# Kernel tuning notes

Measured on AMD Instinct MI355X. Metric: run time of the kernel, lower is better.

The kernel has to match this reference:

```python
import jax, jax.numpy as jnp
import numpy as np

HEADS = 12
DIM = 768
DH = DIM // HEADS


def setup_inputs() -> dict:
    key = jax.random.key(0)
    k1, k2 = jax.random.split(key)
    z = jax.random.normal(k1, (4, 2048, DIM), dtype=jnp.float32)
    # nn.Linear(dim, 3*dim, bias=False): weight shape [3*dim, dim], y = z @ W.T
    W_qkv = jax.random.normal(k2, (3 * DIM, DIM), dtype=jnp.float32) * (1.0 / np.sqrt(DIM))
    return {"z": z, "W_qkv": W_qkv}


def reference(z, W_qkv):
    b, n, d = z.shape
    qkv = jnp.einsum('bnd,ed->bne', z, W_qkv)  # [b, n, 3*dim]
    # last dim layout is (headNum, m, Dh) per the einops pattern '(headNum m Dh)'
    qkv = qkv.reshape(b, n, HEADS, 3, DH)
    q = jnp.transpose(qkv[:, :, :, 0, :], (0, 2, 1, 3))  # [b, h, n, Dh]
    k = jnp.transpose(qkv[:, :, :, 1, :], (0, 2, 1, 3))
    v = jnp.transpose(qkv[:, :, :, 2, :], (0, 2, 1, 3))
    scores = jnp.einsum('bhqd,bhkd->bhqk', q, k) / np.sqrt(DH).astype(np.float32)
    A = jax.nn.softmax(scores, axis=-1)  # full [b, h, n, n] matrix, as in source
    out = jnp.einsum('bhqk,bhkd->bhqd', A, v)  # [b, h, n, Dh]
    return jnp.transpose(out, (0, 2, 1, 3)).reshape(b, n, d)
```

## Files before the change

### kernel.cpp

```cpp
#include <hip/hip_runtime.h>
#include <hip/hip_bf16.h>
#include <stdint.h>


typedef __attribute__((ext_vector_type(8))) short bf8_t;
typedef __attribute__((ext_vector_type(4))) float f4_t;

__device__ __forceinline__ unsigned short f2bf(float f) {
  union { float f; unsigned u; } x; x.f = f;
  return (unsigned short)((x.u + 0x7fffu + ((x.u >> 16) & 1u)) >> 16);
}
__device__ __forceinline__ unsigned cvt_pk_bf16(float lo, float hi) {
  unsigned r;
  asm("v_cvt_pk_bf16_f32 %0, %1, %2" : "=v"(r) : "v"(lo), "v"(hi));
  return r;
}
__device__ __forceinline__ void gload_lds16(const void* g, void* l) {
  __builtin_amdgcn_global_load_lds(
      (const __attribute__((address_space(1))) void*)g,
      (__attribute__((address_space(3))) void*)l, 16, 0, 0);
}

__global__ __launch_bounds__(256) void cvt_kernel(
    const float* __restrict__ Z, const float* __restrict__ W,
    unsigned short* __restrict__ Zb)
{
  const int idx = blockIdx.x * 256 + threadIdx.x;
  const float* src;
  unsigned short* dst;
  int c;
  if (idx < 786432) { src = Z; dst = Zb; c = idx; }
  else              { src = W; dst = Zb + 6291456; c = idx - 786432; }
  const float4 a0 = *(const float4*)(src + (size_t)c * 8);
  const float4 a1 = *(const float4*)(src + (size_t)c * 8 + 4);
  uint4 pk = { cvt_pk_bf16(a0.x, a0.y), cvt_pk_bf16(a0.z, a0.w),
               cvt_pk_bf16(a1.x, a1.y), cvt_pk_bf16(a1.z, a1.w) };
  *(uint4*)(dst + (size_t)c * 8) = pk;
}

__global__ __launch_bounds__(256, 3) void qkv_gemm_kernel(
    const unsigned short* __restrict__ Zb, const unsigned short* __restrict__ Wb,
    unsigned short* __restrict__ qb, unsigned short* __restrict__ kb,
    unsigned short* __restrict__ vt)
{
  __shared__ __align__(16) unsigned short As[128 * 64];
  __shared__ __align__(16) unsigned short Bs[128 * 64];

  const int tid = threadIdx.x;
  const int w    = tid >> 6;
  const int lane = tid & 63;
  const int g    = lane >> 4;
  const int l15  = lane & 15;
  const int bid0 = blockIdx.y * 18 + blockIdx.x;
  const int bid  = (bid0 & 7) * 144 + (bid0 >> 3);
  const int m0 = (bid / 18) * 128;
  const int n0 = (bid % 18) * 128;
  const int wr = w >> 1, wc = w & 1;

  const int arow = w * 32 + (lane >> 3);
  const int achk = ((lane & 7) ^ (lane >> 3)) * 8;
  const unsigned short* za = Zb + (size_t)(m0 + arow) * 768 + achk;
  const unsigned short* wa = Wb + (size_t)(n0 + arow) * 768 + achk;
  unsigned short* const lza = As + w * 32 * 64;
  unsigned short* const lwa = Bs + w * 32 * 64;

  const f4_t zf = {0.f, 0.f, 0.f, 0.f};
  f4_t acc[4][4];
#pragma unroll
  for (int m = 0; m < 4; ++m)
#pragma unroll
    for (int n = 0; n < 4; ++n) acc[m][n] = zf;

  for (int ks = 0; ks < 12; ++ks) {
    __syncthreads();
#pragma unroll
    for (int r = 0; r < 4; ++r) {
      gload_lds16(za + r * 8 * 768, lza + r * 512);
      gload_lds16(wa + r * 8 * 768, lwa + r * 512);
    }
    za += 64; wa += 64;
    __syncthreads();

#pragma unroll
    for (int s = 0; s < 2; ++s) {
      bf8_t af[4], bfr[4];
#pragma unroll
      for (int m = 0; m < 4; ++m) {
        const int row = wr * 64 + m * 16 + l15;
        af[m] = *(const bf8_t*)(As + row * 64 + (((s * 4 + g) ^ (row & 7)) * 8));
      }
#pragma unroll
      for (int n = 0; n < 4; ++n) {
        const int row = wc * 64 + n * 16 + l15;
        bfr[n] = *(const bf8_t*)(Bs + row * 64 + (((s * 4 + g) ^ (row & 7)) * 8));
      }
      __builtin_amdgcn_s_setprio(1);
#pragma unroll
      for (int m = 0; m < 4; ++m)
#pragma unroll
        for (int n = 0; n < 4; ++n)
          acc[m][n] = __builtin_amdgcn_mfma_f32_16x16x32_bf16(af[m], bfr[n], acc[m][n], 0, 0, 0);
      __builtin_amdgcn_s_setprio(0);
    }
  }

  const float QSCALE = 0.18033688011112042f;
#pragma unroll
  for (int m = 0; m < 4; ++m) {
    const int gi  = m0 + wr * 64 + m * 16 + g * 4;
    const int b   = gi >> 11;
    const int tok = gi & 2047;
#pragma unroll
    for (int n = 0; n < 4; ++n) {
      const int e0  = n0 + wc * 64 + n * 16;
      const int h   = e0 / 192;
      const int rem = e0 - h * 192;
      const int mm  = rem >> 6;
      const int dh  = (rem & 63) + l15;
      if (mm == 2) {
        uint2 pk = { cvt_pk_bf16(acc[m][n][0], acc[m][n][1]),
                     cvt_pk_bf16(acc[m][n][2], acc[m][n][3]) };
        const int pos = ((tok >> 5) & 1) * 32 + ((tok >> 2) & 3) * 8
                      + ((tok >> 4) & 1) * 4;
        const size_t vaddr = ((size_t)(b * 12 + h) * 32 + (tok >> 6)) * 4096
                           + dh * 64 + pos;
        *(uint2*)(vt + vaddr) = pk;
      } else {
        unsigned short* buf = mm ? kb : qb;
        const float sc = mm ? 1.0f : QSCALE;
        const size_t base = ((size_t)((b * 12 + h) * 2048 + tok)) * 64 + dh;
#pragma unroll
        for (int j = 0; j < 4; ++j)
          buf[base + (size_t)j * 64] = f2bf(acc[m][n][j] * sc);
      }
    }
  }
}

template <int SPLIT>
__global__ __launch_bounds__(256, 3) void attn_body(
    const unsigned short* __restrict__ qb, const unsigned short* __restrict__ kb,
    const unsigned short* __restrict__ vt, float* __restrict__ out0,
    float* __restrict__ out1, float* __restrict__ lsb)
{
  __shared__ __align__(16) unsigned short Ks[2][64 * 64];
  __shared__ __align__(16) unsigned short Vs[2][64 * 64];

  const int NT = SPLIT ? 16 : 32;
  const int bid = blockIdx.x;
  int bh, qt, half;
  if (SPLIT) {
    const int nb = (bid & 7) * 192 + (bid >> 3);
    qt = nb & 15;
    half = (nb >> 4) & 1;
    bh = nb >> 5;
  } else {
    const int nb = (bid & 7) * 96 + (bid >> 3);
    qt = nb & 15;
    half = 0;
    bh = nb >> 4;
  }
  const int tid = threadIdx.x;
  const int w    = tid >> 6;
  const int lane = tid & 63;
  const int g    = lane >> 4;
  const int l15  = lane & 15;

  const unsigned short* Qh  = qb + (size_t)bh * 2048 * 64;
  const unsigned short* Kh  = kb + (size_t)bh * 2048 * 64 + (size_t)half * 16 * 4096;
  const unsigned short* VTh = vt + (size_t)bh * 32 * 4096 + (size_t)half * 16 * 4096;

  const int qbase = qt * 128 + w * 32;

  bf8_t qfr[2][2];
#pragma unroll
  for (int qq = 0; qq < 2; ++qq)
#pragma unroll
    for (int s = 0; s < 2; ++s)
      qfr[qq][s] = *(const bf8_t*)(Qh + (size_t)(qbase + qq * 16 + l15) * 64 + s * 32 + g * 8);

  const int xk   = l15 & 7;
  const int offA = l15 * 64 + ((g) ^ xk) * 8;
  const int offB = l15 * 64 + ((4 + g) ^ xk) * 8;

  const size_t dmaoff = (size_t)(w * 16 + (lane >> 3)) * 64
                      + ((lane & 7) ^ (lane >> 3)) * 8;
  const unsigned short* ksrc = Kh + dmaoff;
  const unsigned short* vsrc = VTh + dmaoff;
  const int ldsoff = w * 16 * 64;

  gload_lds16(ksrc,                 &Ks[0][ldsoff]);
  gload_lds16(ksrc + 8 * 64,        &Ks[0][ldsoff + 8 * 64]);
  gload_lds16(vsrc,                 &Vs[0][ldsoff]);
  gload_lds16(vsrc + 8 * 64,        &Vs[0][ldsoff + 8 * 64]);
  gload_lds16(ksrc + 4096,          &Ks[1][ldsoff]);
  gload_lds16(ksrc + 4096 + 8 * 64, &Ks[1][ldsoff + 8 * 64]);
  gload_lds16(vsrc + 4096,          &Vs[1][ldsoff]);
  gload_lds16(vsrc + 4096 + 8 * 64, &Vs[1][ldsoff + 8 * 64]);
  __syncthreads();

  const unsigned short* kdma = ksrc + 2 * 4096;
  const unsigned short* vdma = vsrc + 2 * 4096;

  const f4_t m16 = {-16.f, -16.f, -16.f, -16.f};
  const f4_t zf  = {0.f, 0.f, 0.f, 0.f};
  f4_t accO[2][4];
  float lsumP[2] = {0.f, 0.f};
#pragma unroll
  for (int qq = 0; qq < 2; ++qq)
#pragma unroll
    for (int nf = 0; nf < 4; ++nf) accO[qq][nf] = zf;

  for (int t = 0; t < NT; ++t) {
    const int cur = t & 1;
    const unsigned short* pK = &Ks[cur][0];
    const unsigned short* pV = &Vs[cur][0];

    bf8_t ka[4][2];
#pragma unroll
    for (int kf = 0; kf < 4; ++kf) {
      ka[kf][0] = *(const bf8_t*)(pK + offA + kf * 1024);
      ka[kf][1] = *(const bf8_t*)(pK + offB + kf * 1024);
    }
    bf8_t vfr[2][4];
#pragma unroll
    for (int nf = 0; nf < 4; ++nf) {
      vfr[0][nf] = *(const bf8_t*)(pV + offA + nf * 1024);
      vfr[1][nf] = *(const bf8_t*)(pV + offB + nf * 1024);
    }

    __syncthreads();

    if (t < NT - 2) {
      gload_lds16(kdma,          &Ks[cur][ldsoff]);
      gload_lds16(kdma + 8 * 64, &Ks[cur][ldsoff + 8 * 64]);
      gload_lds16(vdma,          &Vs[cur][ldsoff]);
      gload_lds16(vdma + 8 * 64, &Vs[cur][ldsoff + 8 * 64]);
      kdma += 4096; vdma += 4096;
    }

    f4_t accS0[4], accS1[4];
    __builtin_amdgcn_s_setprio(1);
#pragma unroll
    for (int kf = 0; kf < 4; ++kf) {
      f4_t a = __builtin_amdgcn_mfma_f32_16x16x32_bf16(ka[kf][0], qfr[0][0], m16, 0, 0, 0);
      accS0[kf] = __builtin_amdgcn_mfma_f32_16x16x32_bf16(ka[kf][1], qfr[0][1], a, 0, 0, 0);
    }
#pragma unroll
    for (int kf = 0; kf < 4; ++kf) {
      f4_t a = __builtin_amdgcn_mfma_f32_16x16x32_bf16(ka[kf][0], qfr[1][0], m16, 0, 0, 0);
      accS1[kf] = __builtin_amdgcn_mfma_f32_16x16x32_bf16(ka[kf][1], qfr[1][1], a, 0, 0, 0);
    }
    __builtin_amdgcn_s_setprio(0);

#pragma unroll
    for (int qq = 0; qq < 2; ++qq) {
      const f4_t* accS = qq ? accS1 : accS0;
      union { bf8_t v[2]; unsigned uw[8]; } P8;
      float ps = 0.f;
#pragma unroll
      for (int kf = 0; kf < 4; ++kf) {
        const float p0 = __builtin_amdgcn_exp2f(accS[kf][0]);
        const float p1 = __builtin_amdgcn_exp2f(accS[kf][1]);
        const float p2 = __builtin_amdgcn_exp2f(accS[kf][2]);
        const float p3 = __builtin_amdgcn_exp2f(accS[kf][3]);
        ps += (p0 + p1) + (p2 + p3);
        P8.uw[kf * 2]     = cvt_pk_bf16(p0, p1);
        P8.uw[kf * 2 + 1] = cvt_pk_bf16(p2, p3);
      }
      lsumP[qq] += ps;

      __builtin_amdgcn_s_setprio(1);
#pragma unroll
      for (int kk = 0; kk < 2; ++kk)
#pragma unroll
        for (int nf = 0; nf < 4; ++nf)
          accO[qq][nf] = __builtin_amdgcn_mfma_f32_16x16x32_bf16(P8.v[kk], vfr[kk][nf], accO[qq][nf], 0, 0, 0);
      __builtin_amdgcn_s_setprio(0);
    }
  }

  const int b = bh / 12, h = bh - (bh / 12) * 12;
  float* const outP = (SPLIT && half) ? out1 : out0;
#pragma unroll
  for (int qq = 0; qq < 2; ++qq) {
    float ls = lsumP[qq];
    ls += __shfl_xor(ls, 16);
    ls += __shfl_xor(ls, 32);
    if (SPLIT) {
      if (g == 0)
        lsb[((size_t)half * 48 + bh) * 2048 + qbase + qq * 16 + l15] = ls;
#pragma unroll
      for (int nf = 0; nf < 4; ++nf)
#pragma unroll
        for (int j = 0; j < 4; ++j) {
          const int qrow = qbase + qq * 16 + g * 4 + j;
          outP[((size_t)(b * 2048 + qrow)) * 768 + h * 64 + nf * 16 + l15] = accO[qq][nf][j];
        }
    } else {
      const float rl = 1.0f / ls;
      f4_t lv;
#pragma unroll
      for (int j = 0; j < 4; ++j) lv[j] = __shfl(rl, g * 4 + j);
#pragma unroll
      for (int nf = 0; nf < 4; ++nf)
#pragma unroll
        for (int j = 0; j < 4; ++j) {
          const int qrow = qbase + qq * 16 + g * 4 + j;
          outP[((size_t)(b * 2048 + qrow)) * 768 + h * 64 + nf * 16 + l15] = accO[qq][nf][j] * lv[j];
        }
    }
  }
}

__global__ __launch_bounds__(256) void combine_kernel(
    float* __restrict__ out, const float* __restrict__ P1,
    const float* __restrict__ lsb)
{
  const int tid = blockIdx.x * 256 + threadIdx.x;
  const int row = tid >> 3;
  const int dh0 = (tid & 7) * 8;
  const int bh  = row >> 11;
  const int tok = row & 2047;
  const int b   = bh / 12, h = bh - (bh / 12) * 12;

  const float ls = lsb[row] + lsb[(size_t)48 * 2048 + row];
  const float rl = 1.0f / ls;

  const size_t base = ((size_t)(b * 2048 + tok)) * 768 + h * 64 + dh0;
  float4 a0 = *(const float4*)(out + base);
  float4 a1 = *(const float4*)(out + base + 4);
  const float4 b0 = *(const float4*)(P1 + base);
  const float4 b1 = *(const float4*)(P1 + base + 4);
  a0.x = (a0.x + b0.x) * rl; a0.y = (a0.y + b0.y) * rl;
  a0.z = (a0.z + b0.z) * rl; a0.w = (a0.w + b0.w) * rl;
  a1.x = (a1.x + b1.x) * rl; a1.y = (a1.y + b1.y) * rl;
  a1.z = (a1.z + b1.z) * rl; a1.w = (a1.w + b1.w) * rl;
  *(float4*)(out + base)     = a0;
  *(float4*)(out + base + 4) = a1;
}

extern "C" void kernel_launch(void* const* d_in, const int* in_sizes, int n_in,
                              void* d_out, int out_size, void* d_ws, size_t ws_size,
                              hipStream_t stream) {
  (void)in_sizes; (void)n_in; (void)out_size;
  const float* Z = (const float*)d_in[0];
  const float* W = (const float*)d_in[1];
  float* out = (float*)d_out;

  unsigned short* qb = (unsigned short*)d_ws;
  unsigned short* kb = qb + (size_t)48 * 2048 * 64;
  unsigned short* vt = kb + (size_t)48 * 2048 * 64;

  float* P1  = (float*)(vt + (size_t)48 * 32 * 4096);
  float* lsb = P1 + (size_t)48 * 2048 * 64;
  const size_t WS_NEEDED = ((size_t)48 * 2048 * 64 * 2) * 3
                         + (size_t)48 * 2048 * 64 * 4
                         + (size_t)2 * 48 * 2048 * 4;

  unsigned short* Zb = (unsigned short*)d_out;
  unsigned short* Wb = Zb + (size_t)8192 * 768;

  cvt_kernel<<<dim3(3936), 256, 0, stream>>>(Z, W, Zb);
  qkv_gemm_kernel<<<dim3(18, 64), 256, 0, stream>>>(Zb, Wb, qb, kb, vt);

  if (ws_size >= WS_NEEDED) {
    attn_body<1><<<dim3(1536), 256, 0, stream>>>(qb, kb, vt, out, P1, lsb);
    combine_kernel<<<dim3(3072), 256, 0, stream>>>(out, P1, lsb);
  } else {
    attn_body<0><<<dim3(768), 256, 0, stream>>>(qb, kb, vt, out, nullptr, nullptr);
  }
}
```

Baseline: 118.4 us.

## Double per-warp query rows and restructure K/V prefetch to issue before compute

Each warp now handles 64 query rows (4 fragments) instead of 32, so each block covers 256 queries and the grid is halved. Every K/V tile loaded into LDS is therefore reused across twice as many queries. The pipeline changes from a two-tile-ahead prefetch placed after a mid-iteration barrier to a one-tile-ahead prefetch into the other buffer at the top of each iteration, with a single barrier at the end. The trade-off is higher register pressure from the larger accumulators and P buffers under launch_bounds(256,3), which may cause spills or lower occupancy, and a smaller grid of 768 blocks.

```diff
diff --git a/kernel.cpp b/kernel.cpp
--- a/kernel.cpp
+++ b/kernel.cpp
@@ -150,15 +150,11 @@
   const int bid = blockIdx.x;
   int bh, qt, half;
   if (SPLIT) {
-    const int nb = (bid & 7) * 192 + (bid >> 3);
-    qt = nb & 15;
-    half = (nb >> 4) & 1;
-    bh = nb >> 5;
+    const int nb = (bid & 7) * 96 + (bid >> 3);
+    bh = nb >> 4; qt = (nb >> 1) & 7; half = nb & 1;
   } else {
-    const int nb = (bid & 7) * 96 + (bid >> 3);
-    qt = nb & 15;
-    half = 0;
-    bh = nb >> 4;
+    const int nb = (bid & 7) * 48 + (bid >> 3);
+    bh = nb >> 3; qt = nb & 7; half = 0;
   }
   const int tid = threadIdx.x;
   const int w    = tid >> 6;
@@ -170,11 +166,11 @@
   const unsigned short* Kh  = kb + (size_t)bh * 2048 * 64 + (size_t)half * 16 * 4096;
   const unsigned short* VTh = vt + (size_t)bh * 32 * 4096 + (size_t)half * 16 * 4096;
 
-  const int qbase = qt * 128 + w * 32;
-
-  bf8_t qfr[2][2];
-#pragma unroll
-  for (int qq = 0; qq < 2; ++qq)
+  const int qbase = qt * 256 + w * 64;
+
+  bf8_t qfr[4][2];
+#pragma unroll
+  for (int qq = 0; qq < 4; ++qq)
 #pragma unroll
     for (int s = 0; s < 2; ++s)
       qfr[qq][s] = *(const bf8_t*)(Qh + (size_t)(qbase + qq * 16 + l15) * 64 + s * 32 + g * 8);
@@ -189,32 +185,36 @@
   const unsigned short* vsrc = VTh + dmaoff;
   const int ldsoff = w * 16 * 64;
 
-  gload_lds16(ksrc,                 &Ks[0][ldsoff]);
-  gload_lds16(ksrc + 8 * 64,        &Ks[0][ldsoff + 8 * 64]);
-  gload_lds16(vsrc,                 &Vs[0][ldsoff]);
-  gload_lds16(vsrc + 8 * 64,        &Vs[0][ldsoff + 8 * 64]);
-  gload_lds16(ksrc + 4096,          &Ks[1][ldsoff]);
-  gload_lds16(ksrc + 4096 + 8 * 64, &Ks[1][ldsoff + 8 * 64]);
-  gload_lds16(vsrc + 4096,          &Vs[1][ldsoff]);
-  gload_lds16(vsrc + 4096 + 8 * 64, &Vs[1][ldsoff + 8 * 64]);
+  gload_lds16(ksrc,          &Ks[0][ldsoff]);
+  gload_lds16(ksrc + 8 * 64, &Ks[0][ldsoff + 8 * 64]);
+  gload_lds16(vsrc,          &Vs[0][ldsoff]);
+  gload_lds16(vsrc + 8 * 64, &Vs[0][ldsoff + 8 * 64]);
   __syncthreads();
 
-  const unsigned short* kdma = ksrc + 2 * 4096;
-  const unsigned short* vdma = vsrc + 2 * 4096;
+  const unsigned short* kdma = ksrc + 4096;
+  const unsigned short* vdma = vsrc + 4096;
 
   const f4_t m16 = {-16.f, -16.f, -16.f, -16.f};
   const f4_t zf  = {0.f, 0.f, 0.f, 0.f};
-  f4_t accO[2][4];
-  float lsumP[2] = {0.f, 0.f};
-#pragma unroll
-  for (int qq = 0; qq < 2; ++qq)
+  f4_t accO[4][4];
+  float lsumP[4] = {0.f, 0.f, 0.f, 0.f};
+#pragma unroll
+  for (int qq = 0; qq < 4; ++qq)
 #pragma unroll
     for (int nf = 0; nf < 4; ++nf) accO[qq][nf] = zf;
 
   for (int t = 0; t < NT; ++t) {
-    const int cur = t & 1;
+    const int cur = t & 1, nxt = cur ^ 1;
     const unsigned short* pK = &Ks[cur][0];
     const unsigned short* pV = &Vs[cur][0];
+
+    if (t < NT - 1) {
+      gload_lds16(kdma,          &Ks[nxt][ldsoff]);
+      gload_lds16(kdma + 8 * 64, &Ks[nxt][ldsoff + 8 * 64]);
+      gload_lds16(vdma,          &Vs[nxt][ldsoff]);
+      gload_lds16(vdma + 8 * 64, &Vs[nxt][ldsoff + 8 * 64]);
+      kdma += 4096; vdma += 4096;
+    }
 
     bf8_t ka[4][2];
 #pragma unroll
@@ -222,68 +222,70 @@
       ka[kf][0] = *(const bf8_t*)(pK + offA + kf * 1024);
       ka[kf][1] = *(const bf8_t*)(pK + offB + kf * 1024);
     }
+
+    unsigned pw[4][8];
+#pragma unroll
+    for (int qp = 0; qp < 2; ++qp) {
+      f4_t accSa[4], accSb[4];
+      __builtin_amdgcn_s_setprio(1);
+#pragma unroll
+      for (int kf = 0; kf < 4; ++kf) {
+        f4_t a = __builtin_amdgcn_mfma_f32_16x16x32_bf16(ka[kf][0], qfr[qp * 2][0], m16, 0, 0, 0);
+        accSa[kf] = __builtin_amdgcn_mfma_f32_16x16x32_bf16(ka[kf][1], qfr[qp * 2][1], a, 0, 0, 0);
+      }
+#pragma unroll
+      for (int kf = 0; kf < 4; ++kf) {
+        f4_t a = __builtin_amdgcn_mfma_f32_16x16x32_bf16(ka[kf][0], qfr[qp * 2 + 1][0], m16, 0, 0, 0);
+        accSb[kf] = __builtin_amdgcn_mfma_f32_16x16x32_bf16(ka[kf][1], qfr[qp * 2 + 1][1], a, 0, 0, 0);
+      }
+      __builtin_amdgcn_s_setprio(0);
+
+#pragma unroll
+      for (int qh = 0; qh < 2; ++qh) {
+        const int qq = qp * 2 + qh;
+        const f4_t* accS = qh ? accSb : accSa;
+        float ps = 0.f;
+#pragma unroll
+        for (int kf = 0; kf < 4; ++kf) {
+          const float p0 = __builtin_amdgcn_exp2f(accS[kf][0]);
+          const float p1 = __builtin_amdgcn_exp2f(accS[kf][1]);
+          const float p2 = __builtin_amdgcn_exp2f(accS[kf][2]);
+          const float p3 = __builtin_amdgcn_exp2f(accS[kf][3]);
+          ps += (p0 + p1) + (p2 + p3);
+          pw[qq][kf * 2]     = cvt_pk_bf16(p0, p1);
+          pw[qq][kf * 2 + 1] = cvt_pk_bf16(p2, p3);
+        }
+        lsumP[qq] += ps;
+      }
+    }
+
     bf8_t vfr[2][4];
 #pragma unroll
     for (int nf = 0; nf < 4; ++nf) {
       vfr[0][nf] = *(const bf8_t*)(pV + offA + nf * 1024);
       vfr[1][nf] = *(const bf8_t*)(pV + offB + nf * 1024);
     }
+    __builtin_amdgcn_s_setprio(1);
+#pragma unroll
+    for (int qq = 0; qq < 4; ++qq) {
+      union { bf8_t v[2]; unsigned u[8]; } pa;
+#pragma unroll
+      for (int i = 0; i < 8; ++i) pa.u[i] = pw[qq][i];
+#pragma unroll
+      for (int kk = 0; kk < 2; ++kk)
+#pragma unroll
+        for (int nf = 0; nf < 4; ++nf)
+          accO[qq][nf] = __builtin_amdgcn_mfma_f32_16x16x32_bf16(pa.v[kk], vfr[kk][nf], accO[qq][nf], 0, 0, 0);
+    }
+    __builtin_amdgcn_s_setprio(0);
 
     __syncthreads();
-
-    if (t < NT - 2) {
-      gload_lds16(kdma,          &Ks[cur][ldsoff]);
-      gload_lds16(kdma + 8 * 64, &Ks[cur][ldsoff + 8 * 64]);
-      gload_lds16(vdma,          &Vs[cur][ldsoff]);
-      gload_lds16(vdma + 8 * 64, &Vs[cur][ldsoff + 8 * 64]);
-      kdma += 4096; vdma += 4096;
-    }
-
-    f4_t accS0[4], accS1[4];
-    __builtin_amdgcn_s_setprio(1);
-#pragma unroll
-    for (int kf = 0; kf < 4; ++kf) {
-      f4_t a = __builtin_amdgcn_mfma_f32_16x16x32_bf16(ka[kf][0], qfr[0][0], m16, 0, 0, 0);
-      accS0[kf] = __builtin_amdgcn_mfma_f32_16x16x32_bf16(ka[kf][1], qfr[0][1], a, 0, 0, 0);
-    }
-#pragma unroll
-    for (int kf = 0; kf < 4; ++kf) {
-      f4_t a = __builtin_amdgcn_mfma_f32_16x16x32_bf16(ka[kf][0], qfr[1][0], m16, 0, 0, 0);
-      accS1[kf] = __builtin_amdgcn_mfma_f32_16x16x32_bf16(ka[kf][1], qfr[1][1], a, 0, 0, 0);
-    }
-    __builtin_amdgcn_s_setprio(0);
-
-#pragma unroll
-    for (int qq = 0; qq < 2; ++qq) {
-      const f4_t* accS = qq ? accS1 : accS0;
-      union { bf8_t v[2]; unsigned uw[8]; } P8;
-      float ps = 0.f;
-#pragma unroll
-      for (int kf = 0; kf < 4; ++kf) {
-        const float p0 = __builtin_amdgcn_exp2f(accS[kf][0]);
-        const float p1 = __builtin_amdgcn_exp2f(accS[kf][1]);
-        const float p2 = __builtin_amdgcn_exp2f(accS[kf][2]);
-        const float p3 = __builtin_amdgcn_exp2f(accS[kf][3]);
-        ps += (p0 + p1) + (p2 + p3);
-        P8.uw[kf * 2]     = cvt_pk_bf16(p0, p1);
-        P8.uw[kf * 2 + 1] = cvt_pk_bf16(p2, p3);
-      }
-      lsumP[qq] += ps;
-
-      __builtin_amdgcn_s_setprio(1);
-#pragma unroll
-      for (int kk = 0; kk < 2; ++kk)
-#pragma unroll
-        for (int nf = 0; nf < 4; ++nf)
-          accO[qq][nf] = __builtin_amdgcn_mfma_f32_16x16x32_bf16(P8.v[kk], vfr[kk][nf], accO[qq][nf], 0, 0, 0);
-      __builtin_amdgcn_s_setprio(0);
-    }
   }
 
   const int b = bh / 12, h = bh - (bh / 12) * 12;
   float* const outP = (SPLIT && half) ? out1 : out0;
 #pragma unroll
-  for (int qq = 0; qq < 2; ++qq) {
+  for (int qq = 0; qq < 4; ++qq) {
     float ls = lsumP[qq];
     ls += __shfl_xor(ls, 16);
     ls += __shfl_xor(ls, 32);
@@ -365,9 +367,9 @@
   qkv_gemm_kernel<<<dim3(18, 64), 256, 0, stream>>>(Zb, Wb, qb, kb, vt);
 
   if (ws_size >= WS_NEEDED) {
-    attn_body<1><<<dim3(1536), 256, 0, stream>>>(qb, kb, vt, out, P1, lsb);
+    attn_body<1><<<dim3(768), 256, 0, stream>>>(qb, kb, vt, out, P1, lsb);
     combine_kernel<<<dim3(3072), 256, 0, stream>>>(out, P1, lsb);
   } else {
-    attn_body<0><<<dim3(768), 256, 0, stream>>>(qb, kb, vt, out, nullptr, nullptr);
-  }
-}
+    attn_body<0><<<dim3(384), 256, 0, stream>>>(qb, kb, vt, out, nullptr, nullptr);
+  }
+}
```

Result: slower. 162.5 us (+37.3%).
